# Optimization experiments

Measured on AMD Instinct MI355X. Metric: run time of the kernel, lower is better.

## Reference

```python
import jax, jax.numpy as jnp
import numpy as np

NUM_LEVELS = 3
B, T, D, H = 512, 2048, 64, 32


def _uni(k, shape, fan_in):
    s = 1.0 / np.sqrt(fan_in)
    return jax.random.uniform(k, shape, jnp.float32, -s, s)


def setup_inputs() -> dict:
    key = jax.random.key(0)
    ks = jax.random.split(key, 10)
    lw = jnp.linspace(1.0, float(NUM_LEVELS), NUM_LEVELS)
    lw = lw / lw.sum()
    return {
        "latent_ys": jax.random.normal(ks[0], (B, T, D), jnp.float32),
        "Wx": _uni(ks[1], (D, H), D), "bx": _uni(ks[2], (H,), D),
        "Wu": _uni(ks[3], (D, H), D), "bu": _uni(ks[4], (H,), D),
        "Ws": _uni(ks[5], (2 * H, 1), 2 * H), "bs": _uni(ks[6], (1,), 2 * H),
        "level_weights": lw,
        "Wf": _uni(ks[7], (2 * D, D), 2 * D), "bf": _uni(ks[8], (D,), 2 * D),
        "gamma": jnp.ones((D,), jnp.float32),
        "beta": jnp.zeros((D,), jnp.float32),
    }


def reference(latent_ys, Wx, bx, Wu, bu, Ws, bs, level_weights, Wf, bf, gamma, beta):
    Bn, Tn, Dn = latent_ys.shape
    x_repr = latent_ys[:, 0, :]          # (B,D)
    u_repr = latent_ys.mean(axis=1)       # (B,D)

    # Eq. 8-9 attention: score_net is linear on concat, so S[i,j] = ex_i.w1 + eu_j.w2 + b
    ex = x_repr @ Wx + bx                 # (B,H)
    eu = u_repr @ Wu + bu                 # (B,H)
    Hn = ex.shape[-1]
    S = (ex @ Ws[:Hn, 0])[:, None] + (eu @ Ws[Hn:, 0])[None, :] + bs[0]
    eye = jnp.eye(Bn, dtype=bool)
    S = jnp.where(eye, -jnp.inf, S)
    weights = jax.nn.softmax(S, axis=-1)  # (B,B), diag = 0

    # pyramidal sort (Algorithm 1), vectorized over the batch dim
    other = ~eye
    active = other
    dt = latent_ys.dtype
    levels = []
    for _ in range(NUM_LEVELS - 1):
        cnt = active.sum(-1, keepdims=True).astype(dt)                         # (B,1)
        asum = jnp.sum(jnp.where(active, weights, 0.0), -1, keepdims=True)      # (B,1)
        mean_val = asum / jnp.maximum(cnt, 1.0)
        lower = active & (weights <= mean_val)                                  # (B,B)
        lcnt = lower.sum(-1).astype(dt)[:, None]                                # (B,1)
        lsum = lower.astype(dt) @ u_repr                                        # (B,D)
        levels.append(jnp.where(lcnt > 0, lsum / jnp.maximum(lcnt, 1.0), 0.0))
        active = active & ~lower
    acnt = active.sum(-1).astype(dt)[:, None]
    asum_r = active.astype(dt) @ u_repr
    top_idx = jnp.argmax(jnp.where(other, weights, -1.0), axis=-1)              # (B,)
    fallback = u_repr[top_idx]
    levels.append(jnp.where(acnt > 0, asum_r / jnp.maximum(acnt, 1.0), fallback))
    level_reprs = jnp.stack(levels, axis=1)                                     # (B,L,D)

    cross = jnp.einsum('bld,l->bd', level_reprs, level_weights)                 # (B,D)
    # fusion Linear on concat([latent_ys, cross]) split into two GEMMs
    fused = latent_ys @ Wf[:Dn] + (cross @ Wf[Dn:] + bf)[:, None, :]           # (B,T,D)
    y = fused + latent_ys
    mu = y.mean(-1, keepdims=True)
    var = y.var(-1, keepdims=True)
    return gamma * (y - mu) * jax.lax.rsqrt(var + 1e-5) + beta
```

## Files before the change

kernel.cpp:

```cpp
#include <hip/hip_runtime.h>

typedef unsigned short ushort_t;
typedef __attribute__((ext_vector_type(8))) short short8;
typedef __attribute__((ext_vector_type(4))) float f32x4;

#define BB 512
#define TT 2048
#define DD 64

__device__ __forceinline__ ushort_t f2b(float f) {
    union { float f; unsigned int i; } v; v.f = f;
    unsigned int u = v.i;
    unsigned int r = (u + 0x7fffu + ((u >> 16) & 1u)) >> 16;
    return (ushort_t)r;
}

__global__ __launch_bounds__(1024) void k_umean(const float* __restrict__ lat,
                                                float* __restrict__ u) {
    int b = blockIdx.x;
    int tid = threadIdx.x;
    int cg = tid & 15;
    int rs = tid >> 4;
    const float* base = lat + (size_t)b * TT * DD;
    float acc[4] = {0.f, 0.f, 0.f, 0.f};
#pragma unroll 4
    for (int k = 0; k < 32; k++) {
        int r = rs + 64 * k;
        float4 vv = *reinterpret_cast<const float4*>(base + (size_t)r * DD + cg * 4);
        acc[0] += vv.x; acc[1] += vv.y; acc[2] += vv.z; acc[3] += vv.w;
    }
    __shared__ float sm[64][64];
#pragma unroll
    for (int j = 0; j < 4; j++) sm[rs][cg * 4 + j] = acc[j];
    __syncthreads();
    {
        int col = tid & 63, g = tid >> 6;
        float p = 0.0f;
#pragma unroll
        for (int k = 0; k < 4; k++) p += sm[g + 16 * k][col];
        sm[g][col] = p;
    }
    __syncthreads();
    if (tid < 64) {
        float tot = 0.0f;
#pragma unroll
        for (int g = 0; g < 16; g++) tot += sm[g][tid];
        u[(size_t)b * DD + tid] = tot * (1.0f / (float)TT);
    }
}

__global__ __launch_bounds__(512) void k_logits(const float* __restrict__ u,
                                                const float* __restrict__ Wu,
                                                const float* __restrict__ Ws,
                                                float* __restrict__ E,
                                                float* __restrict__ miscf,
                                                int* __restrict__ misci) {
    __shared__ float v[64];
    __shared__ float rv[512];
    __shared__ int ri[512];
    int tid = threadIdx.x;
    if (tid < 64) {
        float s = 0.0f;
        for (int h = 0; h < 32; h++) s += Wu[tid * 32 + h] * Ws[32 + h];
        v[tid] = s;
    }
    __syncthreads();
    float bj = 0.0f;
    for (int d = 0; d < 64; d++) bj += u[(size_t)tid * DD + d] * v[d];
    rv[tid] = bj; ri[tid] = tid;
    __syncthreads();
    for (int off = 256; off > 0; off >>= 1) {
        if (tid < off) {
            float v2 = rv[tid + off]; int i2 = ri[tid + off];
            if (v2 > rv[tid] || (v2 == rv[tid] && i2 < ri[tid])) { rv[tid] = v2; ri[tid] = i2; }
        }
        __syncthreads();
    }
    float maxb = rv[0]; int j1 = ri[0];
    __syncthreads();
    float e = expf(bj - maxb);
    E[tid] = e;
    rv[tid] = e;
    __syncthreads();
    for (int off = 256; off > 0; off >>= 1) {
        if (tid < off) rv[tid] += rv[tid + off];
        __syncthreads();
    }
    float Z = rv[0];
    __syncthreads();
    rv[tid] = (tid == j1) ? -3.4e38f : bj; ri[tid] = tid;
    __syncthreads();
    for (int off = 256; off > 0; off >>= 1) {
        if (tid < off) {
            float v2 = rv[tid + off]; int i2 = ri[tid + off];
            if (v2 > rv[tid] || (v2 == rv[tid] && i2 < ri[tid])) { rv[tid] = v2; ri[tid] = i2; }
        }
        __syncthreads();
    }
    if (tid == 0) { miscf[0] = Z; misci[1] = j1; misci[2] = ri[0]; }
}

__global__ __launch_bounds__(256) void k_levels(const float* __restrict__ u,
                                                const float* __restrict__ E,
                                                const float* __restrict__ miscf,
                                                const int* __restrict__ misci,
                                                const float* __restrict__ lw,
                                                const float* __restrict__ Wf,
                                                const float* __restrict__ bfv,
                                                float* __restrict__ cbias) {
    int i = blockIdx.x;
    int tid = threadIdx.x;
    __shared__ float w[512];
    __shared__ signed char lvl[512];
    __shared__ float r1[256], r2[256], r3[256];
    __shared__ float crossS[64];
    __shared__ float lr[4][3][64];

    float Z = miscf[0];
    float denom = Z - E[i];
    for (int j = tid; j < 512; j += 256) w[j] = (j == i) ? 0.0f : (E[j] / denom);
    __syncthreads();
    float p = 0.0f;
    for (int j = tid; j < 512; j += 256) p += w[j];
    r1[tid] = p;
    __syncthreads();
    for (int off = 128; off > 0; off >>= 1) {
        if (tid < off) r1[tid] += r1[tid + off];
        __syncthreads();
    }
    float mean0 = r1[0] / 511.0f;
    __syncthreads();
    float pa = 0.0f, ca = 0.0f, c1 = 0.0f;
    for (int j = tid; j < 512; j += 256) {
        if (j != i) {
            float wj = w[j];
            if (wj <= mean0) c1 += 1.0f;
            else { pa += wj; ca += 1.0f; }
        }
    }
    r1[tid] = pa; r2[tid] = ca; r3[tid] = c1;
    __syncthreads();
    for (int off = 128; off > 0; off >>= 1) {
        if (tid < off) { r1[tid] += r1[tid + off]; r2[tid] += r2[tid + off]; r3[tid] += r3[tid + off]; }
        __syncthreads();
    }
    float asum1 = r1[0], cact = r2[0], cnt1 = r3[0];
    float mean1 = asum1 / fmaxf(cact, 1.0f);
    __syncthreads();
    float c2 = 0.0f;
    for (int j = tid; j < 512; j += 256) {
        signed char l;
        if (j == i) l = -1;
        else {
            float wj = w[j];
            if (wj <= mean0) l = 0;
            else if (wj <= mean1) { l = 1; c2 += 1.0f; }
            else l = 2;
        }
        lvl[j] = l;
    }
    r1[tid] = c2;
    __syncthreads();
    for (int off = 128; off > 0; off >>= 1) {
        if (tid < off) r1[tid] += r1[tid + off];
        __syncthreads();
    }
    float cnt2 = r1[0];
    float cnt3 = cact - cnt2;
    __syncthreads();
    int d = tid & 63, g = tid >> 6;
    float a0 = 0.0f, a1 = 0.0f, a2 = 0.0f;
    for (int j = g; j < 512; j += 4) {
        signed char l = lvl[j];
        float uv = u[(size_t)j * DD + d];
        if (l == 0) a0 += uv;
        else if (l == 1) a1 += uv;
        else if (l == 2) a2 += uv;
    }
    lr[g][0][d] = a0; lr[g][1][d] = a1; lr[g][2][d] = a2;
    __syncthreads();
    if (tid < 64) {
        float s0 = 0.0f, s1 = 0.0f, s2 = 0.0f;
#pragma unroll
        for (int gg = 0; gg < 4; gg++) { s0 += lr[gg][0][tid]; s1 += lr[gg][1][tid]; s2 += lr[gg][2][tid]; }
        int j1 = misci[1], j2 = misci[2];
        int fb = (j1 == i) ? j2 : j1;
        float L1 = (cnt1 > 0.0f) ? s0 / cnt1 : 0.0f;
        float L2 = (cnt2 > 0.0f) ? s1 / cnt2 : 0.0f;
        float L3 = (cnt3 > 0.0f) ? s2 / cnt3 : u[(size_t)fb * DD + tid];
        crossS[tid] = lw[0] * L1 + lw[1] * L2 + lw[2] * L3;
    }
    __syncthreads();
    if (tid < 64) {
        int n = tid;
        float s = 0.0f;
        for (int dd = 0; dd < 64; dd++) s += crossS[dd] * Wf[(64 + dd) * 64 + n];
        cbias[(size_t)i * DD + n] = s + bfv[n];
    }
}

__global__ __launch_bounds__(256) void k_fused(const float* __restrict__ lat,
                                               const float* __restrict__ Wf,
                                               const float* __restrict__ cbias,
                                               const float* __restrict__ gamma,
                                               const float* __restrict__ beta,
                                               float* __restrict__ out) {
    int tid = threadIdx.x;
    int lane = tid & 63, wv = tid >> 6;
    int lo = lane & 15, quad = lane >> 4;
    long wid = (long)blockIdx.x * 4 + wv;

    short8 bfr[4][2];
#pragma unroll
    for (int c = 0; c < 4; c++) {
        int n = 16 * c + lo;
#pragma unroll
        for (int s = 0; s < 2; s++) {
            short8 t;
#pragma unroll
            for (int j = 0; j < 8; j++) {
                int k = 32 * s + 8 * quad + j;
                float vv = Wf[k * 64 + n] + (k == n ? 1.0f : 0.0f);
                t[j] = (short)f2b(vv);
            }
            bfr[c][s] = t;
        }
    }
    float ga[4], be[4], cb[4];
    int b = (int)(wid >> 5);
#pragma unroll
    for (int c = 0; c < 4; c++) {
        int n = 16 * c + lo;
        ga[c] = gamma[n];
        be[c] = beta[n];
        cb[c] = cbias[(size_t)b * DD + n];
    }

    for (int t4 = 0; t4 < 4; t4++) {
        long row0 = (wid * 4 + t4) * 16;
        const float* ap = lat + (size_t)(row0 + lo) * DD + quad * 8;
        float4 f0 = *reinterpret_cast<const float4*>(ap);
        float4 f1 = *reinterpret_cast<const float4*>(ap + 4);
        float4 f2 = *reinterpret_cast<const float4*>(ap + 32);
        float4 f3 = *reinterpret_cast<const float4*>(ap + 36);
        short8 a0, a1;
        a0[0] = (short)f2b(f0.x); a0[1] = (short)f2b(f0.y);
        a0[2] = (short)f2b(f0.z); a0[3] = (short)f2b(f0.w);
        a0[4] = (short)f2b(f1.x); a0[5] = (short)f2b(f1.y);
        a0[6] = (short)f2b(f1.z); a0[7] = (short)f2b(f1.w);
        a1[0] = (short)f2b(f2.x); a1[1] = (short)f2b(f2.y);
        a1[2] = (short)f2b(f2.z); a1[3] = (short)f2b(f2.w);
        a1[4] = (short)f2b(f3.x); a1[5] = (short)f2b(f3.y);
        a1[6] = (short)f2b(f3.z); a1[7] = (short)f2b(f3.w);

        f32x4 acc[4];
#pragma unroll
        for (int c = 0; c < 4; c++) { acc[c] = (f32x4){0.f, 0.f, 0.f, 0.f}; }
#pragma unroll
        for (int c = 0; c < 4; c++) {
            acc[c] = __builtin_amdgcn_mfma_f32_16x16x32_bf16(a0, bfr[c][0], acc[c], 0, 0, 0);
            acc[c] = __builtin_amdgcn_mfma_f32_16x16x32_bf16(a1, bfr[c][1], acc[c], 0, 0, 0);
        }
        float y[4][4];
#pragma unroll
        for (int c = 0; c < 4; c++)
#pragma unroll
            for (int r = 0; r < 4; r++) y[c][r] = acc[c][r] + cb[c];
#pragma unroll
        for (int r = 0; r < 4; r++) {
            float s = y[0][r] + y[1][r] + y[2][r] + y[3][r];
            float q = y[0][r] * y[0][r] + y[1][r] * y[1][r] + y[2][r] * y[2][r] + y[3][r] * y[3][r];
#pragma unroll
            for (int m = 1; m < 16; m <<= 1) {
                s += __shfl_xor(s, m, 64);
                q += __shfl_xor(q, m, 64);
            }
            float mean = s * (1.0f / 64.0f);
            float var = q * (1.0f / 64.0f) - mean * mean;
            float rstd = rsqrtf(var + 1e-5f);
            long row = row0 + quad * 4 + r;
#pragma unroll
            for (int c = 0; c < 4; c++) {
                float o = ga[c] * (y[c][r] - mean) * rstd + be[c];
                out[(size_t)row * DD + 16 * c + lo] = o;
            }
        }
    }
}

extern "C" void kernel_launch(void* const* d_in, const int* in_sizes, int n_in,
                              void* d_out, int out_size, void* d_ws, size_t ws_size,
                              hipStream_t stream) {
    const float* lat   = (const float*)d_in[0];
    const float* Wu    = (const float*)d_in[3];
    const float* Ws    = (const float*)d_in[5];
    const float* lw    = (const float*)d_in[7];
    const float* Wf    = (const float*)d_in[8];
    const float* bfv   = (const float*)d_in[9];
    const float* gamma = (const float*)d_in[10];
    const float* beta  = (const float*)d_in[11];
    float* out = (float*)d_out;

    char* ws = (char*)d_ws;
    float* u     = (float*)(ws);
    float* E     = (float*)(ws + 131072);
    float* miscf = (float*)(ws + 133120);
    int*   misci = (int*)(ws + 133120);
    float* cbias = (float*)(ws + 133376);

    k_umean<<<BB, 1024, 0, stream>>>(lat, u);
    k_logits<<<1, 512, 0, stream>>>(u, Wu, Ws, E, miscf, misci);
    k_levels<<<BB, 256, 0, stream>>>(u, E, miscf, misci, lw, Wf, bfv, cbias);
    k_fused<<<4096, 256, 0, stream>>>(lat, Wf, cbias, gamma, beta, out);
}
```

Before: 568.9 us.

## Fold logit dot into mean kernel and use wave-shuffle reductions

Moves the per-row logit dot product (u·(Wu·Ws2)) into the mean kernel and replaces the single-block 512-thread logits kernel with a one-wave stats kernel built on shuffle reductions. The levels kernel swaps its shared-memory tree reductions for wave shuffles with a small cross-wave array, and uses float4 loads across 16 row groups for the level sums. The intent is to remove many __syncthreads barriers and serial reduction steps in the small kernels. The large kernels that dominate total time are unchanged, so the possible gain is limited to these small kernels.

```diff
diff --git a/kernel.cpp b/kernel.cpp
--- a/kernel.cpp
+++ b/kernel.cpp
@@ -16,7 +16,10 @@
 }
 
 __global__ __launch_bounds__(1024) void k_umean(const float* __restrict__ lat,
-                                                float* __restrict__ u) {
+                                                const float* __restrict__ Wu,
+                                                const float* __restrict__ Ws,
+                                                float* __restrict__ u,
+                                                float* __restrict__ bj) {
     int b = blockIdx.x;
     int tid = threadIdx.x;
     int cg = tid & 15;
@@ -45,59 +48,62 @@
         float tot = 0.0f;
 #pragma unroll
         for (int g = 0; g < 16; g++) tot += sm[g][tid];
-        u[(size_t)b * DD + tid] = tot * (1.0f / (float)TT);
-    }
-}
-
-__global__ __launch_bounds__(512) void k_logits(const float* __restrict__ u,
-                                                const float* __restrict__ Wu,
-                                                const float* __restrict__ Ws,
-                                                float* __restrict__ E,
-                                                float* __restrict__ miscf,
-                                                int* __restrict__ misci) {
-    __shared__ float v[64];
-    __shared__ float rv[512];
-    __shared__ int ri[512];
-    int tid = threadIdx.x;
-    if (tid < 64) {
-        float s = 0.0f;
-        for (int h = 0; h < 32; h++) s += Wu[tid * 32 + h] * Ws[32 + h];
-        v[tid] = s;
-    }
-    __syncthreads();
-    float bj = 0.0f;
-    for (int d = 0; d < 64; d++) bj += u[(size_t)tid * DD + d] * v[d];
-    rv[tid] = bj; ri[tid] = tid;
-    __syncthreads();
-    for (int off = 256; off > 0; off >>= 1) {
-        if (tid < off) {
-            float v2 = rv[tid + off]; int i2 = ri[tid + off];
-            if (v2 > rv[tid] || (v2 == rv[tid] && i2 < ri[tid])) { rv[tid] = v2; ri[tid] = i2; }
-        }
-        __syncthreads();
-    }
-    float maxb = rv[0]; int j1 = ri[0];
-    __syncthreads();
-    float e = expf(bj - maxb);
-    E[tid] = e;
-    rv[tid] = e;
-    __syncthreads();
-    for (int off = 256; off > 0; off >>= 1) {
-        if (tid < off) rv[tid] += rv[tid + off];
-        __syncthreads();
-    }
-    float Z = rv[0];
-    __syncthreads();
-    rv[tid] = (tid == j1) ? -3.4e38f : bj; ri[tid] = tid;
-    __syncthreads();
-    for (int off = 256; off > 0; off >>= 1) {
-        if (tid < off) {
-            float v2 = rv[tid + off]; int i2 = ri[tid + off];
-            if (v2 > rv[tid] || (v2 == rv[tid] && i2 < ri[tid])) { rv[tid] = v2; ri[tid] = i2; }
-        }
-        __syncthreads();
-    }
-    if (tid == 0) { miscf[0] = Z; misci[1] = j1; misci[2] = ri[0]; }
+        float um = tot * (1.0f / (float)TT);
+        u[(size_t)b * DD + tid] = um;
+        float vv = 0.0f;
+#pragma unroll
+        for (int h = 0; h < 32; h++) vv += Wu[tid * 32 + h] * Ws[32 + h];
+        float p = um * vv;
+#pragma unroll
+        for (int m = 1; m < 64; m <<= 1) p += __shfl_xor(p, m, 64);
+        if (tid == 0) bj[b] = p;
+    }
+}
+
+__global__ __launch_bounds__(64) void k_stats(const float* __restrict__ bj,
+                                              float* __restrict__ E,
+                                              float* __restrict__ miscf,
+                                              int* __restrict__ misci) {
+    int lane = threadIdx.x;
+    float vals[8];
+#pragma unroll
+    for (int k = 0; k < 8; k++) vals[k] = bj[lane + 64 * k];
+    float mx = vals[0]; int mi = lane;
+#pragma unroll
+    for (int k = 1; k < 8; k++) {
+        int j = lane + 64 * k;
+        if (vals[k] > mx) { mx = vals[k]; mi = j; }
+    }
+#pragma unroll
+    for (int m = 1; m < 64; m <<= 1) {
+        float om = __shfl_xor(mx, m, 64);
+        int oi = __shfl_xor(mi, m, 64);
+        if (om > mx || (om == mx && oi < mi)) { mx = om; mi = oi; }
+    }
+    int j1 = mi; float maxb = mx;
+    float mx2 = -3.4e38f; int mi2 = 0x7fffffff;
+#pragma unroll
+    for (int k = 0; k < 8; k++) {
+        int j = lane + 64 * k;
+        float t = (j == j1) ? -3.4e38f : vals[k];
+        if (t > mx2 || (t == mx2 && j < mi2)) { mx2 = t; mi2 = j; }
+    }
+#pragma unroll
+    for (int m = 1; m < 64; m <<= 1) {
+        float om = __shfl_xor(mx2, m, 64);
+        int oi = __shfl_xor(mi2, m, 64);
+        if (om > mx2 || (om == mx2 && oi < mi2)) { mx2 = om; mi2 = oi; }
+    }
+    float zs = 0.0f;
+#pragma unroll
+    for (int k = 0; k < 8; k++) {
+        float e = expf(vals[k] - maxb);
+        E[lane + 64 * k] = e;
+        zs += e;
+    }
+#pragma unroll
+    for (int m = 1; m < 64; m <<= 1) zs += __shfl_xor(zs, m, 64);
+    if (lane == 0) { miscf[0] = zs; misci[1] = j1; misci[2] = mi2; }
 }
 
 __global__ __launch_bounds__(256) void k_levels(const float* __restrict__ u,
@@ -110,79 +116,86 @@
                                                 float* __restrict__ cbias) {
     int i = blockIdx.x;
     int tid = threadIdx.x;
-    __shared__ float w[512];
+    int lane = tid & 63, wv = tid >> 6;
     __shared__ signed char lvl[512];
-    __shared__ float r1[256], r2[256], r3[256];
+    __shared__ float red[16];
+    __shared__ __align__(16) float lr[16][3][64];
     __shared__ float crossS[64];
-    __shared__ float lr[4][3][64];
 
     float Z = miscf[0];
-    float denom = Z - E[i];
-    for (int j = tid; j < 512; j += 256) w[j] = (j == i) ? 0.0f : (E[j] / denom);
-    __syncthreads();
-    float p = 0.0f;
-    for (int j = tid; j < 512; j += 256) p += w[j];
-    r1[tid] = p;
-    __syncthreads();
-    for (int off = 128; off > 0; off >>= 1) {
-        if (tid < off) r1[tid] += r1[tid + off];
-        __syncthreads();
-    }
-    float mean0 = r1[0] / 511.0f;
-    __syncthreads();
+    float Ei = E[i];
+    float denom = Z - Ei;
+    int jA = tid, jB = tid + 256;
+    float wA = (jA == i) ? 0.0f : (E[jA] / denom);
+    float wB = (jB == i) ? 0.0f : (E[jB] / denom);
+
+    float s = wA + wB;
+#pragma unroll
+    for (int m = 1; m < 64; m <<= 1) s += __shfl_xor(s, m, 64);
+    if (lane == 0) red[wv] = s;
+    __syncthreads();
+    float mean0 = (red[0] + red[1] + red[2] + red[3]) * (1.0f / 511.0f);
+
     float pa = 0.0f, ca = 0.0f, c1 = 0.0f;
-    for (int j = tid; j < 512; j += 256) {
-        if (j != i) {
-            float wj = w[j];
-            if (wj <= mean0) c1 += 1.0f;
-            else { pa += wj; ca += 1.0f; }
-        }
-    }
-    r1[tid] = pa; r2[tid] = ca; r3[tid] = c1;
-    __syncthreads();
-    for (int off = 128; off > 0; off >>= 1) {
-        if (tid < off) { r1[tid] += r1[tid + off]; r2[tid] += r2[tid + off]; r3[tid] += r3[tid + off]; }
-        __syncthreads();
-    }
-    float asum1 = r1[0], cact = r2[0], cnt1 = r3[0];
+    if (jA != i) { if (wA <= mean0) c1 += 1.0f; else { pa += wA; ca += 1.0f; } }
+    if (jB != i) { if (wB <= mean0) c1 += 1.0f; else { pa += wB; ca += 1.0f; } }
+#pragma unroll
+    for (int m = 1; m < 64; m <<= 1) {
+        pa += __shfl_xor(pa, m, 64);
+        ca += __shfl_xor(ca, m, 64);
+        c1 += __shfl_xor(c1, m, 64);
+    }
+    if (lane == 0) { red[4 + wv] = pa; red[8 + wv] = ca; red[12 + wv] = c1; }
+    __syncthreads();
+    float asum1 = red[4] + red[5] + red[6] + red[7];
+    float cact  = red[8] + red[9] + red[10] + red[11];
+    float cnt1  = red[12] + red[13] + red[14] + red[15];
     float mean1 = asum1 / fmaxf(cact, 1.0f);
-    __syncthreads();
+
     float c2 = 0.0f;
-    for (int j = tid; j < 512; j += 256) {
-        signed char l;
-        if (j == i) l = -1;
-        else {
-            float wj = w[j];
-            if (wj <= mean0) l = 0;
-            else if (wj <= mean1) { l = 1; c2 += 1.0f; }
-            else l = 2;
-        }
-        lvl[j] = l;
-    }
-    r1[tid] = c2;
-    __syncthreads();
-    for (int off = 128; off > 0; off >>= 1) {
-        if (tid < off) r1[tid] += r1[tid + off];
-        __syncthreads();
-    }
-    float cnt2 = r1[0];
+    signed char lA, lB;
+    if (jA == i) lA = -1;
+    else if (wA <= mean0) lA = 0;
+    else if (wA <= mean1) { lA = 1; c2 += 1.0f; }
+    else lA = 2;
+    if (jB == i) lB = -1;
+    else if (wB <= mean0) lB = 0;
+    else if (wB <= mean1) { lB = 1; c2 += 1.0f; }
+    else lB = 2;
+    lvl[jA] = lA; lvl[jB] = lB;
+#pragma unroll
+    for (int m = 1; m < 64; m <<= 1) c2 += __shfl_xor(c2, m, 64);
+    if (lane == 0) red[wv] = c2;
+    __syncthreads();
+    float cnt2 = red[0] + red[1] + red[2] + red[3];
     float cnt3 = cact - cnt2;
-    __syncthreads();
-    int d = tid & 63, g = tid >> 6;
-    float a0 = 0.0f, a1 = 0.0f, a2 = 0.0f;
-    for (int j = g; j < 512; j += 4) {
-        signed char l = lvl[j];
-        float uv = u[(size_t)j * DD + d];
-        if (l == 0) a0 += uv;
-        else if (l == 1) a1 += uv;
-        else if (l == 2) a2 += uv;
-    }
-    lr[g][0][d] = a0; lr[g][1][d] = a1; lr[g][2][d] = a2;
-    __syncthreads();
+
+    int jg = tid >> 4;
+    int d4 = (tid & 15) << 2;
+    float4 a0 = make_float4(0.f, 0.f, 0.f, 0.f);
+    float4 a1 = make_float4(0.f, 0.f, 0.f, 0.f);
+    float4 a2 = make_float4(0.f, 0.f, 0.f, 0.f);
+#pragma unroll 8
+    for (int j = jg; j < 512; j += 16) {
+        int l = lvl[j];
+        float4 uv = *reinterpret_cast<const float4*>(u + (size_t)j * DD + d4);
+        if (l == 0) { a0.x += uv.x; a0.y += uv.y; a0.z += uv.z; a0.w += uv.w; }
+        else if (l == 1) { a1.x += uv.x; a1.y += uv.y; a1.z += uv.z; a1.w += uv.w; }
+        else if (l == 2) { a2.x += uv.x; a2.y += uv.y; a2.z += uv.z; a2.w += uv.w; }
+    }
+    *reinterpret_cast<float4*>(&lr[jg][0][d4]) = a0;
+    *reinterpret_cast<float4*>(&lr[jg][1][d4]) = a1;
+    *reinterpret_cast<float4*>(&lr[jg][2][d4]) = a2;
+    __syncthreads();
+
     if (tid < 64) {
         float s0 = 0.0f, s1 = 0.0f, s2 = 0.0f;
 #pragma unroll
-        for (int gg = 0; gg < 4; gg++) { s0 += lr[gg][0][tid]; s1 += lr[gg][1][tid]; s2 += lr[gg][2][tid]; }
+        for (int g2 = 0; g2 < 16; g2++) {
+            s0 += lr[g2][0][tid];
+            s1 += lr[g2][1][tid];
+            s2 += lr[g2][2][tid];
+        }
         int j1 = misci[1], j2 = misci[2];
         int fb = (j1 == i) ? j2 : j1;
         float L1 = (cnt1 > 0.0f) ? s0 / cnt1 : 0.0f;
@@ -193,9 +206,9 @@
     __syncthreads();
     if (tid < 64) {
         int n = tid;
-        float s = 0.0f;
-        for (int dd = 0; dd < 64; dd++) s += crossS[dd] * Wf[(64 + dd) * 64 + n];
-        cbias[(size_t)i * DD + n] = s + bfv[n];
+        float sacc = 0.0f;
+        for (int dd = 0; dd < 64; dd++) sacc += crossS[dd] * Wf[(64 + dd) * 64 + n];
+        cbias[(size_t)i * DD + n] = sacc + bfv[n];
     }
 }
 
@@ -303,13 +316,14 @@
 
     char* ws = (char*)d_ws;
     float* u     = (float*)(ws);
-    float* E     = (float*)(ws + 131072);
-    float* miscf = (float*)(ws + 133120);
-    int*   misci = (int*)(ws + 133120);
-    float* cbias = (float*)(ws + 133376);
-
-    k_umean<<<BB, 1024, 0, stream>>>(lat, u);
-    k_logits<<<1, 512, 0, stream>>>(u, Wu, Ws, E, miscf, misci);
+    float* bjv   = (float*)(ws + 131072);
+    float* E     = (float*)(ws + 133120);
+    float* miscf = (float*)(ws + 135168);
+    int*   misci = (int*)(ws + 135168);
+    float* cbias = (float*)(ws + 135424);
+
+    k_umean<<<BB, 1024, 0, stream>>>(lat, Wu, Ws, u, bjv);
+    k_stats<<<1, 64, 0, stream>>>(bjv, E, miscf, misci);
     k_levels<<<BB, 256, 0, stream>>>(u, E, miscf, misci, lw, Wf, bfv, cbias);
     k_fused<<<4096, 256, 0, stream>>>(lat, Wf, cbias, gamma, beta, out);
 }
```

Result: faster. 539.6 us (-5.1%).
